# Kernel tuning notes

Measured on AMD Instinct MI355X. Metric: run time of the kernel, lower is better.

Reference implementation:

```python
import jax, jax.numpy as jnp
import numpy as np

EPS = 1e-5


def spmm(rows, cols, vals, x):
    # x: (B, C, V); y[b,c,v] = sum_{e: rows[e]==v} vals[e] * x[b,c,cols[e]]
    B, C, V = x.shape
    xt = x.reshape(B * C, V).T                      # (V, B*C)
    msg = vals[:, None] * xt[cols]                  # (E, B*C)
    y = jax.ops.segment_sum(msg, rows, num_segments=V)
    return y.T.reshape(B, C, V)


def cheb_conv(x, W, b, rows, cols, vals):
    # W: (K, Cin, Cout); Chebyshev recurrence over node dim
    K = W.shape[0]
    Tk = [x]
    if K > 1:
        Tk.append(spmm(rows, cols, vals, x))
    for _ in range(2, K):
        Tk.append(2.0 * spmm(rows, cols, vals, Tk[-1]) - Tk[-2])
    T = jnp.stack(Tk)                               # (K, B, Cin, V)
    out = jnp.einsum('kbiv,kio->bov', T, W)
    if b is not None:
        out = out + b[None, :, None]
    return out


def bn(x, g, be):
    # BatchNorm1d training-mode stats over (batch, nodes) per channel
    m = jnp.mean(x, axis=(0, 2), keepdims=True)
    v = jnp.var(x, axis=(0, 2), keepdims=True)
    return (x - m) * jax.lax.rsqrt(v + EPS) * g[None, :, None] + be[None, :, None]


def res_block(x, rows, cols, vals, ga, bea, Wa, ba, gb, beb, Wb, bb, Ws=None):
    xn = bn(x, ga, bea)
    out = cheb_conv(xn, Wa, ba, rows, cols, vals)
    out = bn(jax.nn.relu(out), gb, beb)
    out = cheb_conv(out, Wb, bb, rows, cols, vals)
    sc = xn if Ws is None else cheb_conv(xn, Ws, None, rows, cols, vals)
    return jax.nn.relu(out + sc)


def setup_inputs() -> dict:
    key = jax.random.key(0)
    ks = iter(jax.random.split(key, 40))
    V, E, B, K = 50000, 800000, 8, 4
    d = {}
    d['x'] = jax.random.normal(next(ks), (B, 16, V), dtype=jnp.float32)
    d['lap_rows'] = jax.random.randint(next(ks), (E,), 0, V, dtype=jnp.int32)
    d['lap_cols'] = jax.random.randint(next(ks), (E,), 0, V, dtype=jnp.int32)
    d['lap_vals'] = jax.random.normal(next(ks), (E,), dtype=jnp.float32) * 0.05

    def w(shape, scale=0.1):
        return jax.random.normal(next(ks), shape, dtype=jnp.float32) * scale

    d['W_in'], d['b_in'] = w((K, 16, 32)), w((32,))
    # block 1: 32 -> [32] -> 32 (identity shortcut)
    d['g1a'], d['be1a'] = jnp.ones(32), jnp.zeros(32)
    d['W1a'], d['b1a'] = w((K, 32, 32)), w((32,))
    d['g1b'], d['be1b'] = jnp.ones(32), jnp.zeros(32)
    d['W1b'], d['b1b'] = w((K, 32, 32)), w((32,))
    # block 2: 32 -> [64] -> 64 (ChebConv K=1 shortcut, no bias)
    d['g2a'], d['be2a'] = jnp.ones(32), jnp.zeros(32)
    d['W2a'], d['b2a'] = w((K, 32, 64)), w((64,))
    d['g2b'], d['be2b'] = jnp.ones(64), jnp.zeros(64)
    d['W2b'], d['b2b'] = w((K, 64, 64)), w((64,))
    d['W2s'] = w((1, 32, 64))
    # block 3: 64 -> [64] -> 64 (identity shortcut)
    d['g3a'], d['be3a'] = jnp.ones(64), jnp.zeros(64)
    d['W3a'], d['b3a'] = w((K, 64, 64)), w((64,))
    d['g3b'], d['be3b'] = jnp.ones(64), jnp.zeros(64)
    d['W3b'], d['b3b'] = w((K, 64, 64)), w((64,))
    # output head
    d['g_out'], d['be_out'] = jnp.ones(64), jnp.zeros(64)
    d['W_out'], d['b_out'] = w((K, 64, 10)), w((10,))
    return d


def reference(x, lap_rows, lap_cols, lap_vals,
              W_in, b_in,
              g1a, be1a, W1a, b1a, g1b, be1b, W1b, b1b,
              g2a, be2a, W2a, b2a, g2b, be2b, W2b, b2b, W2s,
              g3a, be3a, W3a, b3a, g3b, be3b, W3b, b3b,
              g_out, be_out, W_out, b_out):
    r, c, v = lap_rows, lap_cols, lap_vals
    out = jax.nn.relu(cheb_conv(x, W_in, b_in, r, c, v))
    out = res_block(out, r, c, v, g1a, be1a, W1a, b1a, g1b, be1b, W1b, b1b)
    out = res_block(out, r, c, v, g2a, be2a, W2a, b2a, g2b, be2b, W2b, b2b, W2s)
    out = res_block(out, r, c, v, g3a, be3a, W3a, b3a, g3b, be3b, W3b, b3b)
    out = bn(out, g_out, be_out)
    out = jax.nn.relu(cheb_conv(out, W_out, b_out, r, c, v))
    pooled = jnp.max(out, axis=2)                   # global max pool over nodes -> (B, 10)
    return jax.nn.log_softmax(pooled, axis=1)
```

## Files before the change

### kernel.cpp

```cpp
#include <hip/hip_runtime.h>
#include <hip/hip_bf16.h>
#include <hip/hip_fp16.h>

__global__ void hist_kernel(const int* __restrict__ rows, int* __restrict__ counts, int E) {
    int i = blockIdx.x * blockDim.x + threadIdx.x;
    if (i < E) atomicAdd(&counts[rows[i]], 1);
}

__global__ void chunk_sum_kernel(const int* __restrict__ counts, int* __restrict__ chunk_sums, int V) {
    __shared__ int sh[256];
    int t = threadIdx.x;
    int i = blockIdx.x * 256 + t;
    sh[t] = (i < V) ? counts[i] : 0;
    __syncthreads();
    for (int st = 128; st > 0; st >>= 1) {
        if (t < st) sh[t] += sh[t + st];
        __syncthreads();
    }
    if (t == 0) chunk_sums[blockIdx.x] = sh[0];
}

__global__ void scan_chunks_kernel(int* __restrict__ cs, int n) {
    __shared__ int wsum[4];
    int t = threadIdx.x, lane = t & 63, w = t >> 6;
    int orig = (t < n) ? cs[t] : 0;
    int x = orig;
    #pragma unroll
    for (int d = 1; d < 64; d <<= 1) {
        int y = __shfl_up(x, d);
        if (lane >= d) x += y;
    }
    if (lane == 63) wsum[w] = x;
    __syncthreads();
    int wo = 0;
    for (int j = 0; j < w; ++j) wo += wsum[j];
    if (t < n) cs[t] = wo + x - orig;
}

__global__ void scan_final_kernel(const int* __restrict__ counts, const int* __restrict__ chunk_off,
                                  int* __restrict__ row_ptr, int V) {
    __shared__ int wsum[4];
    int t = threadIdx.x, lane = t & 63, w = t >> 6;
    int i = blockIdx.x * 256 + t;
    int x = (i < V) ? counts[i] : 0;
    #pragma unroll
    for (int d = 1; d < 64; d <<= 1) {
        int y = __shfl_up(x, d);
        if (lane >= d) x += y;
    }
    if (lane == 63) wsum[w] = x;
    __syncthreads();
    int wo = 0;
    for (int j = 0; j < w; ++j) wo += wsum[j];
    if (i < V) row_ptr[i + 1] = chunk_off[blockIdx.x] + wo + x;
    if (i == 0) row_ptr[0] = 0;
}

__global__ void init_cursor_kernel(const int* __restrict__ row_ptr, int* __restrict__ cursor, int V) {
    int i = blockIdx.x * blockDim.x + threadIdx.x;
    if (i < V) cursor[i] = row_ptr[i];
}

__global__ void scatter_kernel(const int* __restrict__ rows, const int* __restrict__ cols,
                               const float* __restrict__ vals, int* __restrict__ cursor,
                               int* __restrict__ cols_s, float* __restrict__ vals_s, int E) {
    int i = blockIdx.x * blockDim.x + threadIdx.x;
    if (i < E) {
        int r = rows[i];
        int p = atomicAdd(&cursor[r], 1);
        cols_s[p] = cols[i];
        vals_s[p] = vals[i];
    }
}

__global__ void sort_rows_kernel(const int* __restrict__ row_ptr, int* cols, float* vals, int V) {
    int v = blockIdx.x * blockDim.x + threadIdx.x;
    if (v >= V) return;
    int e0 = row_ptr[v], e1 = row_ptr[v + 1];
    for (int i = e0 + 1; i < e1; ++i) {
        int c = cols[i];
        unsigned xb = __float_as_uint(vals[i]);
        int j = i - 1;
        while (j >= e0) {
            int cj = cols[j];
            unsigned vj = __float_as_uint(vals[j]);
            if (cj > c || (cj == c && vj > xb)) {
                cols[j + 1] = cj; vals[j + 1] = __uint_as_float(vj);
                --j;
            } else break;
        }
        cols[j + 1] = c;
        vals[j + 1] = __uint_as_float(xb);
    }
}

__global__ void transpose_in_kernel(const float* __restrict__ x, __half* __restrict__ X, int V) {
    int total = V * 128;
    for (int i = blockIdx.x * blockDim.x + threadIdx.x; i < total; i += gridDim.x * blockDim.x) {
        int v = i >> 7;
        int t = i & 127;
        X[i] = __float2half(x[t * V + v]);
    }
}

template <int VPT> struct PackT;
template <> struct PackT<1> { using T = float;  };
template <> struct PackT<2> { using T = float2; };
template <> struct PackT<4> { using T = float4; };

template <int VPT>
__global__ __launch_bounds__(256) void spmm2_kernel(
    const int* __restrict__ row_ptr, const int* __restrict__ cols,
    const float* __restrict__ vals, const __half2* __restrict__ src,
    __half2* dst, const __half2* prev, int V) {
    using T = typename PackT<VPT>::T;
    union U { T raw; __half2 h[VPT]; };
    int lane = threadIdx.x & 63;
    int v = (blockIdx.x << 2) | (threadIdx.x >> 6);
    if (v >= V) return;
    const int W = VPT * 64;
    const size_t row = (size_t)v * W + lane * VPT;

    float pr[2 * VPT];
    bool hasp = (prev != nullptr);
    if (hasp) {
        U pv; pv.raw = *(const T*)(prev + row);
        #pragma unroll
        for (int j = 0; j < VPT; ++j) {
            float2 f = __half22float2(pv.h[j]);
            pr[2 * j] = f.x; pr[2 * j + 1] = f.y;
        }
    }
    float acc[2 * VPT];
    #pragma unroll
    for (int j = 0; j < 2 * VPT; ++j) acc[j] = 0.f;

    int e0 = row_ptr[v], e1 = row_ptr[v + 1];
    int e = e0;
    for (; e + 8 <= e1; e += 8) {
        int   c[8]; float w[8]; U g[8];
        #pragma unroll
        for (int k = 0; k < 8; ++k) { c[k] = cols[e + k]; w[k] = vals[e + k]; }
        #pragma unroll
        for (int k = 0; k < 8; ++k)
            g[k].raw = *(const T*)(src + (size_t)c[k] * W + lane * VPT);
        #pragma unroll
        for (int k = 0; k < 8; ++k) {
            #pragma unroll
            for (int j = 0; j < VPT; ++j) {
                float2 f = __half22float2(g[k].h[j]);
                acc[2*j] += w[k] * f.x; acc[2*j+1] += w[k] * f.y;
            }
        }
    }
    for (; e + 4 <= e1; e += 4) {
        int   c[4]; float w[4]; U g[4];
        #pragma unroll
        for (int k = 0; k < 4; ++k) { c[k] = cols[e + k]; w[k] = vals[e + k]; }
        #pragma unroll
        for (int k = 0; k < 4; ++k)
            g[k].raw = *(const T*)(src + (size_t)c[k] * W + lane * VPT);
        #pragma unroll
        for (int k = 0; k < 4; ++k) {
            #pragma unroll
            for (int j = 0; j < VPT; ++j) {
                float2 f = __half22float2(g[k].h[j]);
                acc[2*j] += w[k] * f.x; acc[2*j+1] += w[k] * f.y;
            }
        }
    }
    for (; e < e1; ++e) {
        int c = cols[e]; float wv = vals[e];
        U g; g.raw = *(const T*)(src + (size_t)c * W + lane * VPT);
        #pragma unroll
        for (int j = 0; j < VPT; ++j) {
            float2 f = __half22float2(g.h[j]);
            acc[2*j] += wv * f.x; acc[2*j+1] += wv * f.y;
        }
    }
    if (hasp) {
        #pragma unroll
        for (int j = 0; j < 2 * VPT; ++j) acc[j] = 2.f * acc[j] - pr[j];
    }
    U o;
    #pragma unroll
    for (int j = 0; j < VPT; ++j) o.h[j] = __floats2half2_rn(acc[2*j], acc[2*j+1]);
    *(T*)(dst + row) = o.raw;
}

template <int CIN, int COUT>
__global__ __launch_bounds__(256) void combine_kernel(
    const __half* T0, const __half* T1, const __half* T2, const __half* T3,
    const float* __restrict__ W, const float* __restrict__ bias,
    const __half* res, const __half* sc, const float* __restrict__ Wsc,
    __half* out, int relu, int V) {
    const int CSC = 32;
    int g = blockIdx.x * 256 + threadIdx.x;
    int n = g >> 3, b = g & 7;
    if (n >= V) return;
    size_t ib = (size_t)n * 8 * CIN + (size_t)b * CIN;

    float acc[COUT];
    if (bias) {
        #pragma unroll
        for (int c = 0; c < COUT; ++c) acc[c] = bias[c];
    } else {
        #pragma unroll
        for (int c = 0; c < COUT; ++c) acc[c] = 0.f;
    }

    const __half* Ts[4] = {T0, T1, T2, T3};
    #pragma unroll
    for (int k = 0; k < 4; ++k) {
        const __half2* xr = (const __half2*)(Ts[k] + ib);
        const float* Wk = W + (size_t)k * CIN * COUT;
        for (int q = 0; q < CIN / 2; ++q) {
            float2 x = __half22float2(xr[q]);
            const float* w0 = Wk + (2 * q) * COUT;
            const float* w1 = Wk + (2 * q + 1) * COUT;
            #pragma unroll
            for (int c = 0; c < COUT; ++c) acc[c] = fmaf(x.x, w0[c], acc[c]);
            #pragma unroll
            for (int c = 0; c < COUT; ++c) acc[c] = fmaf(x.y, w1[c], acc[c]);
        }
    }
    if (sc) {
        const __half2* xr = (const __half2*)(sc + (size_t)n * 8 * CSC + (size_t)b * CSC);
        for (int q = 0; q < CSC / 2; ++q) {
            float2 x = __half22float2(xr[q]);
            const float* w0 = Wsc + (2 * q) * COUT;
            const float* w1 = Wsc + (2 * q + 1) * COUT;
            #pragma unroll
            for (int c = 0; c < COUT; ++c) acc[c] = fmaf(x.x, w0[c], acc[c]);
            #pragma unroll
            for (int c = 0; c < COUT; ++c) acc[c] = fmaf(x.y, w1[c], acc[c]);
        }
    }
    size_t ob = (size_t)n * 8 * COUT + (size_t)b * COUT;
    if (res) {
        const __half2* rr = (const __half2*)(res + ob);
        #pragma unroll
        for (int c = 0; c < COUT / 2; ++c) {
            float2 f = __half22float2(rr[c]);
            acc[2 * c] += f.x; acc[2 * c + 1] += f.y;
        }
    }
    if (relu) {
        #pragma unroll
        for (int c = 0; c < COUT; ++c) acc[c] = fmaxf(acc[c], 0.f);
    }
    __half2* ro = (__half2*)(out + ob);
    #pragma unroll
    for (int c = 0; c < COUT / 2; ++c)
        ro[c] = __floats2half2_rn(acc[2 * c], acc[2 * c + 1]);
}

__global__ void bn_stats_part_kernel(const __half* __restrict__ x, int C, int relu_in,
                                     float* __restrict__ part, size_t N) {
    __shared__ float s_sum[256];
    __shared__ float s_sq[256];
    int t = threadIdx.x;
    size_t i0 = (size_t)blockIdx.x * 256 + t;
    size_t step = (size_t)gridDim.x * 256;
    float s = 0.f, q = 0.f;
    for (size_t i = i0; i < N; i += step) {
        float v = __half2float(x[i]);
        if (relu_in) v = fmaxf(v, 0.f);
        s += v; q += v * v;
    }
    s_sum[t] = s; s_sq[t] = q;
    __syncthreads();
    for (int st = 128; st >= C; st >>= 1) {
        if (t < st) { s_sum[t] += s_sum[t + st]; s_sq[t] += s_sq[t + st]; }
        __syncthreads();
    }
    if (t < C) {
        part[blockIdx.x * 128 + t]     = s_sum[t];
        part[blockIdx.x * 128 + C + t] = s_sq[t];
    }
}

__global__ void bn_reduce_kernel(const float* __restrict__ part, int nblk,
                                 const float* __restrict__ g, const float* __restrict__ be,
                                 float* __restrict__ ss, int C, float invN) {
    int c = threadIdx.x;
    if (c < C) {
        float s = 0.f, q = 0.f;
        for (int b = 0; b < nblk; ++b) {
            s += part[b * 128 + c];
            q += part[b * 128 + C + c];
        }
        float m = s * invN;
        float var = q * invN - m * m;
        float sc = g[c] * rsqrtf(var + 1e-5f);
        ss[c] = sc;
        ss[C + c] = be[c] - m * sc;
    }
}

__global__ void affine_h_kernel(__half* x, const float* __restrict__ ss, int C,
                                int relu_in, size_t N) {
    size_t stride = (size_t)gridDim.x * blockDim.x;
    for (size_t i = (size_t)blockIdx.x * blockDim.x + threadIdx.x; i < N; i += stride) {
        int c = (int)(i & (size_t)(C - 1));
        float v = __half2float(x[i]);
        if (relu_in) v = fmaxf(v, 0.f);
        x[i] = __float2half(v * ss[c] + ss[C + c]);
    }
}

__global__ void maxpool_h_kernel(const __half* __restrict__ x, float* __restrict__ pooled, int V) {
    __shared__ float red[256];
    int o = blockIdx.x;
    float m = 0.f;
    for (int v = threadIdx.x; v < V; v += 256)
        m = fmaxf(m, __half2float(x[(size_t)v * 80 + o]));
    red[threadIdx.x] = m;
    __syncthreads();
    for (int st = 128; st > 0; st >>= 1) {
        if (threadIdx.x < st) red[threadIdx.x] = fmaxf(red[threadIdx.x], red[threadIdx.x + st]);
        __syncthreads();
    }
    if (threadIdx.x == 0) pooled[o] = red[0];
}

__global__ void lsm_kernel(const float* __restrict__ pooled, float* __restrict__ out) {
    int b = threadIdx.x;
    if (b < 8) {
        float m = -1e30f;
        for (int c = 0; c < 10; ++c) m = fmaxf(m, pooled[b * 10 + c]);
        float s = 0.f;
        for (int c = 0; c < 10; ++c) s += expf(pooled[b * 10 + c] - m);
        float l = logf(s);
        for (int c = 0; c < 10; ++c)
            out[b * 10 + c] = pooled[b * 10 + c] - m - l;
    }
}

__global__ void encode_kernel(float* out, float val) {
    int i = threadIdx.x;
    if (i < 80) out[i] = val;
}

extern "C" void kernel_launch(void* const* d_in, const int* in_sizes, int n_in,
                              void* d_out, int out_size, void* d_ws, size_t ws_size,
                              hipStream_t stream) {
    (void)in_sizes; (void)n_in; (void)out_size;
    const int V = 50000, E = 800000;
    const int NCH = (V + 255) / 256;
    const int SB = 256;

    auto al = [](size_t x) { return (x + 255) & ~(size_t)255; };
    const size_t FB = al((size_t)V * 512 * sizeof(__half));
    const size_t need = 5 * FB + al((V + 1) * 4) + al(V * 4) + al(E * 4) + al(E * 4)
                      + al(SB * 128 * 4) + al(8 * 128 * 4) + al(80 * 4) + al(NCH * 4);
    if (ws_size < need) {
        encode_kernel<<<1, 128, 0, stream>>>((float*)d_out, (float)(ws_size >> 20));
        return;
    }

    const float* x_in = (const float*)d_in[0];
    const int* rows   = (const int*)d_in[1];
    const int* colsi  = (const int*)d_in[2];
    const float* lvals = (const float*)d_in[3];
    const float* W_in = (const float*)d_in[4];
    const float* b_in = (const float*)d_in[5];
    const float* g1a = (const float*)d_in[6],  *be1a = (const float*)d_in[7];
    const float* W1a = (const float*)d_in[8],  *b1a  = (const float*)d_in[9];
    const float* g1b = (const float*)d_in[10], *be1b = (const float*)d_in[11];
    const float* W1b = (const float*)d_in[12], *b1b  = (const float*)d_in[13];
    const float* g2a = (const float*)d_in[14], *be2a = (const float*)d_in[15];
    const float* W2a = (const float*)d_in[16], *b2a  = (const float*)d_in[17];
    const float* g2b = (const float*)d_in[18], *be2b = (const float*)d_in[19];
    const float* W2b = (const float*)d_in[20], *b2b  = (const float*)d_in[21];
    const float* W2s = (const float*)d_in[22];
    const float* g3a = (const float*)d_in[23], *be3a = (const float*)d_in[24];
    const float* W3a = (const float*)d_in[25], *b3a  = (const float*)d_in[26];
    const float* g3b = (const float*)d_in[27], *be3b = (const float*)d_in[28];
    const float* W3b = (const float*)d_in[29], *b3b  = (const float*)d_in[30];
    const float* g_o = (const float*)d_in[31], *be_o = (const float*)d_in[32];
    const float* W_o = (const float*)d_in[33], *b_o  = (const float*)d_in[34];

    char* wp = (char*)d_ws;
    auto take = [&](size_t bytes) -> void* { void* p = (void*)wp; wp += al(bytes); return p; };
    __half* P0 = (__half*)take(FB);
    __half* P1 = (__half*)take(FB);
    __half* P2 = (__half*)take(FB);
    __half* P3 = (__half*)take(FB);
    __half* P4 = (__half*)take(FB);
    int* row_ptr  = (int*)take((V + 1) * sizeof(int));
    int* cursor   = (int*)take(V * sizeof(int));
    int* cols_s   = (int*)take(E * sizeof(int));
    float* vals_s = (float*)take(E * sizeof(float));
    float* part   = (float*)take(SB * 128 * sizeof(float));
    float* aff    = (float*)take(8 * 128 * sizeof(float));
    float* pooled = (float*)take(80 * sizeof(float));
    int* chunks   = (int*)take(NCH * sizeof(int));

    hipMemsetAsync(d_ws, 0, need, stream);

    hist_kernel<<<(E + 255) / 256, 256, 0, stream>>>(rows, cursor, E);
    chunk_sum_kernel<<<NCH, 256, 0, stream>>>(cursor, chunks, V);
    scan_chunks_kernel<<<1, 256, 0, stream>>>(chunks, NCH);
    scan_final_kernel<<<NCH, 256, 0, stream>>>(cursor, chunks, row_ptr, V);
    init_cursor_kernel<<<(V + 255) / 256, 256, 0, stream>>>(row_ptr, cursor, V);
    scatter_kernel<<<(E + 255) / 256, 256, 0, stream>>>(rows, colsi, lvals, cursor, cols_s, vals_s, E);
    sort_rows_kernel<<<(V + 255) / 256, 256, 0, stream>>>(row_ptr, cols_s, vals_s, V);
    transpose_in_kernel<<<4096, 256, 0, stream>>>(x_in, P0, V);

    auto spmm = [&](const __half* src, __half* dst, const __half* prev, int C) {
        int grid = (V + 3) / 4;
        if (C == 16)
            spmm2_kernel<1><<<grid, 256, 0, stream>>>(row_ptr, cols_s, vals_s,
                (const __half2*)src, (__half2*)dst, (const __half2*)prev, V);
        else if (C == 32)
            spmm2_kernel<2><<<grid, 256, 0, stream>>>(row_ptr, cols_s, vals_s,
                (const __half2*)src, (__half2*)dst, (const __half2*)prev, V);
        else
            spmm2_kernel<4><<<grid, 256, 0, stream>>>(row_ptr, cols_s, vals_s,
                (const __half2*)src, (__half2*)dst, (const __half2*)prev, V);
    };
    const int MG = (V * 8 + 255) / 256;
    auto comb = [&](const __half* T0, const __half* T1, const __half* T2, const __half* T3,
                    int Cin, int Cout, const float* W, const float* bias,
                    const __half* res, const __half* sc, const float* Wsc,
                    __half* out, int relu) {
        if (Cin == 16 && Cout == 32)
            combine_kernel<16, 32><<<MG, 256, 0, stream>>>(T0, T1, T2, T3, W, bias, res, sc, Wsc, out, relu, V);
        else if (Cin == 32 && Cout == 32)
            combine_kernel<32, 32><<<MG, 256, 0, stream>>>(T0, T1, T2, T3, W, bias, res, sc, Wsc, out, relu, V);
        else if (Cin == 32 && Cout == 64)
            combine_kernel<32, 64><<<MG, 256, 0, stream>>>(T0, T1, T2, T3, W, bias, res, sc, Wsc, out, relu, V);
        else if (Cin == 64 && Cout == 64)
            combine_kernel<64, 64><<<MG, 256, 0, stream>>>(T0, T1, T2, T3, W, bias, res, sc, Wsc, out, relu, V);
        else
            combine_kernel<64, 10><<<MG, 256, 0, stream>>>(T0, T1, T2, T3, W, bias, res, sc, Wsc, out, relu, V);
    };
    auto stats = [&](const __half* xb, int C, int relu, int slot, const float* g, const float* be) {
        bn_stats_part_kernel<<<SB, 256, 0, stream>>>(xb, C, relu, part, (size_t)V * 8 * C);
        bn_reduce_kernel<<<1, 64, 0, stream>>>(part, SB, g, be, aff + slot * 128, C,
                                               1.f / ((float)V * 8.f));
    };
    auto affine = [&](__half* xb, int C, int relu, int slot) {
        affine_h_kernel<<<2048, 256, 0, stream>>>(xb, aff + slot * 128, C, relu, (size_t)V * 8 * C);
    };
    const __half* NH = nullptr;
    const float*  NF = nullptr;

    spmm(P0, P1, nullptr, 16);
    spmm(P1, P2, P0, 16);
    spmm(P2, P3, P1, 16);
    comb(P0, P1, P2, P3, 16, 32, W_in, b_in, NH, NH, NF, P4, 1);

    stats(P4, 32, 0, 0, g1a, be1a);
    affine(P4, 32, 0, 0);
    spmm(P4, P0, nullptr, 32);
    spmm(P0, P1, P4, 32);
    spmm(P1, P2, P0, 32);
    comb(P4, P0, P1, P2, 32, 32, W1a, b1a, NH, NH, NF, P0, 0);
    stats(P0, 32, 1, 1, g1b, be1b);
    affine(P0, 32, 1, 1);
    spmm(P0, P1, nullptr, 32);
    spmm(P1, P2, P0, 32);
    spmm(P2, P3, P1, 32);
    comb(P0, P1, P2, P3, 32, 32, W1b, b1b, P4, NH, NF, P4, 1);

    stats(P4, 32, 0, 2, g2a, be2a);
    affine(P4, 32, 0, 2);
    spmm(P4, P0, nullptr, 32);
    spmm(P0, P1, P4, 32);
    spmm(P1, P2, P0, 32);
    comb(P4, P0, P1, P2, 32, 64, W2a, b2a, NH, NH, NF, P3, 0);
    stats(P3, 64, 1, 3, g2b, be2b);
    affine(P3, 64, 1, 3);
    spmm(P3, P0, nullptr, 64);
    spmm(P0, P1, P3, 64);
    spmm(P1, P2, P0, 64);
    comb(P3, P0, P1, P2, 64, 64, W2b, b2b, NH, P4, W2s, P0, 1);

    stats(P0, 64, 0, 4, g3a, be3a);
    affine(P0, 64, 0, 4);
    spmm(P0, P1, nullptr, 64);
    spmm(P1, P2, P0, 64);
    spmm(P2, P3, P1, 64);
    comb(P0, P1, P2, P3, 64, 64, W3a, b3a, NH, NH, NF, P1, 0);
    stats(P1, 64, 1, 5, g3b, be3b);
    affine(P1, 64, 1, 5);
    spmm(P1, P2, nullptr, 64);
    spmm(P2, P3, P1, 64);
    spmm(P3, P4, P2, 64);
    comb(P1, P2, P3, P4, 64, 64, W3b, b3b, P0, NH, NF, P1, 1);

    stats(P1, 64, 0, 6, g_o, be_o);
    affine(P1, 64, 0, 6);
    spmm(P1, P0, nullptr, 64);
    spmm(P0, P2, P1, 64);
    spmm(P2, P3, P0, 64);
    comb(P1, P0, P2, P3, 64, 10, W_o, b_o, NH, NH, NF, P4, 1);
    maxpool_h_kernel<<<80, 256, 0, stream>>>(P4, pooled, V);
    lsm_kernel<<<1, 64, 0, stream>>>(pooled, (float*)d_out);
}
```

Baseline: 4.897 ms.

## Process two rows per thread in combine, vectorize affine, split maxpool, trim memset

The combine kernel now computes two batch rows per thread with float4 input loads, so each weight load is reused twice. The affine kernel is vectorized to half2, and maxpool is split across node slices that merge with an integer atomicMax on non-negative floats. Batch-norm stats use more blocks, and the full workspace memset is replaced by zeroing only the cursor and pooled buffers. The costs are higher register pressure in combine and a reliance on pooled values being non-negative.

```diff
diff --git a/kernel.cpp b/kernel.cpp
--- a/kernel.cpp
+++ b/kernel.cpp
@@ -195,64 +195,100 @@
     const __half* res, const __half* sc, const float* __restrict__ Wsc,
     __half* out, int relu, int V) {
     const int CSC = 32;
+    union U4 { float4 raw; __half2 h[4]; };
     int g = blockIdx.x * 256 + threadIdx.x;
-    int n = g >> 3, b = g & 7;
-    if (n >= V) return;
+    int r0 = 2 * g;
+    if (r0 >= V * 8) return;
+    int n = r0 >> 3, b = r0 & 7;
     size_t ib = (size_t)n * 8 * CIN + (size_t)b * CIN;
 
-    float acc[COUT];
-    if (bias) {
-        #pragma unroll
-        for (int c = 0; c < COUT; ++c) acc[c] = bias[c];
-    } else {
-        #pragma unroll
-        for (int c = 0; c < COUT; ++c) acc[c] = 0.f;
+    float acc0[COUT], acc1[COUT];
+    #pragma unroll
+    for (int c = 0; c < COUT; ++c) {
+        float bb = bias ? bias[c] : 0.f;
+        acc0[c] = bb; acc1[c] = bb;
     }
 
     const __half* Ts[4] = {T0, T1, T2, T3};
     #pragma unroll
     for (int k = 0; k < 4; ++k) {
-        const __half2* xr = (const __half2*)(Ts[k] + ib);
+        const float4* rp0 = (const float4*)(Ts[k] + ib);
+        const float4* rp1 = (const float4*)(Ts[k] + ib + CIN);
         const float* Wk = W + (size_t)k * CIN * COUT;
-        for (int q = 0; q < CIN / 2; ++q) {
-            float2 x = __half22float2(xr[q]);
-            const float* w0 = Wk + (2 * q) * COUT;
-            const float* w1 = Wk + (2 * q + 1) * COUT;
+        for (int c4 = 0; c4 < CIN / 8; ++c4) {
+            U4 x0, x1;
+            x0.raw = rp0[c4];
+            x1.raw = rp1[c4];
             #pragma unroll
-            for (int c = 0; c < COUT; ++c) acc[c] = fmaf(x.x, w0[c], acc[c]);
+            for (int s = 0; s < 4; ++s) {
+                int q = c4 * 4 + s;
+                float2 a0 = __half22float2(x0.h[s]);
+                float2 a1 = __half22float2(x1.h[s]);
+                const float* w0 = Wk + (2 * q) * COUT;
+                const float* w1 = Wk + (2 * q + 1) * COUT;
+                #pragma unroll
+                for (int c = 0; c < COUT; ++c) {
+                    float wv0 = w0[c], wv1 = w1[c];
+                    acc0[c] = fmaf(a0.x, wv0, acc0[c]);
+                    acc0[c] = fmaf(a0.y, wv1, acc0[c]);
+                    acc1[c] = fmaf(a1.x, wv0, acc1[c]);
+                    acc1[c] = fmaf(a1.y, wv1, acc1[c]);
+                }
+            }
+        }
+    }
+    if (sc) {
+        size_t sb = (size_t)n * 8 * CSC + (size_t)b * CSC;
+        const float4* sp0 = (const float4*)(sc + sb);
+        const float4* sp1 = (const float4*)(sc + sb + CSC);
+        for (int c4 = 0; c4 < CSC / 8; ++c4) {
+            U4 x0, x1;
+            x0.raw = sp0[c4];
+            x1.raw = sp1[c4];
             #pragma unroll
-            for (int c = 0; c < COUT; ++c) acc[c] = fmaf(x.y, w1[c], acc[c]);
-        }
-    }
-    if (sc) {
-        const __half2* xr = (const __half2*)(sc + (size_t)n * 8 * CSC + (size_t)b * CSC);
-        for (int q = 0; q < CSC / 2; ++q) {
-            float2 x = __half22float2(xr[q]);
-            const float* w0 = Wsc + (2 * q) * COUT;
-            const float* w1 = Wsc + (2 * q + 1) * COUT;
-            #pragma unroll
-            for (int c = 0; c < COUT; ++c) acc[c] = fmaf(x.x, w0[c], acc[c]);
-            #pragma unroll
-            for (int c = 0; c < COUT; ++c) acc[c] = fmaf(x.y, w1[c], acc[c]);
+            for (int s = 0; s < 4; ++s) {
+                int q = c4 * 4 + s;
+                float2 a0 = __half22float2(x0.h[s]);
+                float2 a1 = __half22float2(x1.h[s]);
+                const float* w0 = Wsc + (2 * q) * COUT;
+                const float* w1 = Wsc + (2 * q + 1) * COUT;
+                #pragma unroll
+                for (int c = 0; c < COUT; ++c) {
+                    float wv0 = w0[c], wv1 = w1[c];
+                    acc0[c] = fmaf(a0.x, wv0, acc0[c]);
+                    acc0[c] = fmaf(a0.y, wv1, acc0[c]);
+                    acc1[c] = fmaf(a1.x, wv0, acc1[c]);
+                    acc1[c] = fmaf(a1.y, wv1, acc1[c]);
+                }
+            }
         }
     }
     size_t ob = (size_t)n * 8 * COUT + (size_t)b * COUT;
     if (res) {
-        const __half2* rr = (const __half2*)(res + ob);
+        const __half2* rr0 = (const __half2*)(res + ob);
+        const __half2* rr1 = (const __half2*)(res + ob + COUT);
         #pragma unroll
         for (int c = 0; c < COUT / 2; ++c) {
-            float2 f = __half22float2(rr[c]);
-            acc[2 * c] += f.x; acc[2 * c + 1] += f.y;
+            float2 f0 = __half22float2(rr0[c]);
+            float2 f1 = __half22float2(rr1[c]);
+            acc0[2*c] += f0.x; acc0[2*c+1] += f0.y;
+            acc1[2*c] += f1.x; acc1[2*c+1] += f1.y;
         }
     }
     if (relu) {
         #pragma unroll
-        for (int c = 0; c < COUT; ++c) acc[c] = fmaxf(acc[c], 0.f);
-    }
-    __half2* ro = (__half2*)(out + ob);
-    #pragma unroll
-    for (int c = 0; c < COUT / 2; ++c)
-        ro[c] = __floats2half2_rn(acc[2 * c], acc[2 * c + 1]);
+        for (int c = 0; c < COUT; ++c) {
+            acc0[c] = fmaxf(acc0[c], 0.f);
+            acc1[c] = fmaxf(acc1[c], 0.f);
+        }
+    }
+    __half2* ro0 = (__half2*)(out + ob);
+    __half2* ro1 = (__half2*)(out + ob + COUT);
+    #pragma unroll
+    for (int c = 0; c < COUT / 2; ++c) {
+        ro0[c] = __floats2half2_rn(acc0[2*c], acc0[2*c+1]);
+        ro1[c] = __floats2half2_rn(acc1[2*c], acc1[2*c+1]);
+    }
 }
 
 __global__ void bn_stats_part_kernel(const __half* __restrict__ x, int C, int relu_in,
@@ -299,21 +335,27 @@
 }
 
 __global__ void affine_h_kernel(__half* x, const float* __restrict__ ss, int C,
-                                int relu_in, size_t N) {
+                                int relu_in, size_t N2) {
     size_t stride = (size_t)gridDim.x * blockDim.x;
-    for (size_t i = (size_t)blockIdx.x * blockDim.x + threadIdx.x; i < N; i += stride) {
-        int c = (int)(i & (size_t)(C - 1));
-        float v = __half2float(x[i]);
-        if (relu_in) v = fmaxf(v, 0.f);
-        x[i] = __float2half(v * ss[c] + ss[C + c]);
-    }
-}
-
-__global__ void maxpool_h_kernel(const __half* __restrict__ x, float* __restrict__ pooled, int V) {
+    __half2* x2 = (__half2*)x;
+    for (size_t i = (size_t)blockIdx.x * blockDim.x + threadIdx.x; i < N2; i += stride) {
+        int c0 = (int)((2 * i) & (size_t)(C - 1));
+        float2 f = __half22float2(x2[i]);
+        if (relu_in) { f.x = fmaxf(f.x, 0.f); f.y = fmaxf(f.y, 0.f); }
+        f.x = f.x * ss[c0] + ss[C + c0];
+        f.y = f.y * ss[c0 + 1] + ss[C + c0 + 1];
+        x2[i] = __floats2half2_rn(f.x, f.y);
+    }
+}
+
+__global__ void maxpool_h_kernel(const __half* __restrict__ x, float* pooled, int V, int NS) {
     __shared__ float red[256];
-    int o = blockIdx.x;
+    int o = blockIdx.x % 80;
+    int slice = blockIdx.x / 80;
+    int v0 = (int)((long long)V * slice / NS);
+    int v1 = (int)((long long)V * (slice + 1) / NS);
     float m = 0.f;
-    for (int v = threadIdx.x; v < V; v += 256)
+    for (int v = v0 + threadIdx.x; v < v1; v += 256)
         m = fmaxf(m, __half2float(x[(size_t)v * 80 + o]));
     red[threadIdx.x] = m;
     __syncthreads();
@@ -321,7 +363,7 @@
         if (threadIdx.x < st) red[threadIdx.x] = fmaxf(red[threadIdx.x], red[threadIdx.x + st]);
         __syncthreads();
     }
-    if (threadIdx.x == 0) pooled[o] = red[0];
+    if (threadIdx.x == 0) atomicMax((int*)&pooled[o], __float_as_int(red[0]));
 }
 
 __global__ void lsm_kernel(const float* __restrict__ pooled, float* __restrict__ out) {
@@ -348,12 +390,13 @@
     (void)in_sizes; (void)n_in; (void)out_size;
     const int V = 50000, E = 800000;
     const int NCH = (V + 255) / 256;
-    const int SB = 256;
+    const int SB = 1024;
+    const int NS = 8;
 
     auto al = [](size_t x) { return (x + 255) & ~(size_t)255; };
     const size_t FB = al((size_t)V * 512 * sizeof(__half));
     const size_t need = 5 * FB + al((V + 1) * 4) + al(V * 4) + al(E * 4) + al(E * 4)
-                      + al(SB * 128 * 4) + al(8 * 128 * 4) + al(80 * 4) + al(NCH * 4);
+                      + al((size_t)SB * 128 * 4) + al(8 * 128 * 4) + al(80 * 4) + al(NCH * 4);
     if (ws_size < need) {
         encode_kernel<<<1, 128, 0, stream>>>((float*)d_out, (float)(ws_size >> 20));
         return;
@@ -392,12 +435,13 @@
     int* cursor   = (int*)take(V * sizeof(int));
     int* cols_s   = (int*)take(E * sizeof(int));
     float* vals_s = (float*)take(E * sizeof(float));
-    float* part   = (float*)take(SB * 128 * sizeof(float));
+    float* part   = (float*)take((size_t)SB * 128 * sizeof(float));
     float* aff    = (float*)take(8 * 128 * sizeof(float));
     float* pooled = (float*)take(80 * sizeof(float));
     int* chunks   = (int*)take(NCH * sizeof(int));
 
-    hipMemsetAsync(d_ws, 0, need, stream);
+    hipMemsetAsync(cursor, 0, V * sizeof(int), stream);
+    hipMemsetAsync(pooled, 0, 80 * sizeof(float), stream);
 
     hist_kernel<<<(E + 255) / 256, 256, 0, stream>>>(rows, cursor, E);
     chunk_sum_kernel<<<NCH, 256, 0, stream>>>(cursor, chunks, V);
@@ -420,21 +464,21 @@
             spmm2_kernel<4><<<grid, 256, 0, stream>>>(row_ptr, cols_s, vals_s,
                 (const __half2*)src, (__half2*)dst, (const __half2*)prev, V);
     };
-    const int MG = (V * 8 + 255) / 256;
+    const int MG2 = (V * 8 / 2 + 255) / 256;
     auto comb = [&](const __half* T0, const __half* T1, const __half* T2, const __half* T3,
                     int Cin, int Cout, const float* W, const float* bias,
                     const __half* res, const __half* sc, const float* Wsc,
                     __half* out, int relu) {
         if (Cin == 16 && Cout == 32)
-            combine_kernel<16, 32><<<MG, 256, 0, stream>>>(T0, T1, T2, T3, W, bias, res, sc, Wsc, out, relu, V);
+            combine_kernel<16, 32><<<MG2, 256, 0, stream>>>(T0, T1, T2, T3, W, bias, res, sc, Wsc, out, relu, V);
         else if (Cin == 32 && Cout == 32)
-            combine_kernel<32, 32><<<MG, 256, 0, stream>>>(T0, T1, T2, T3, W, bias, res, sc, Wsc, out, relu, V);
+            combine_kernel<32, 32><<<MG2, 256, 0, stream>>>(T0, T1, T2, T3, W, bias, res, sc, Wsc, out, relu, V);
         else if (Cin == 32 && Cout == 64)
-            combine_kernel<32, 64><<<MG, 256, 0, stream>>>(T0, T1, T2, T3, W, bias, res, sc, Wsc, out, relu, V);
+            combine_kernel<32, 64><<<MG2, 256, 0, stream>>>(T0, T1, T2, T3, W, bias, res, sc, Wsc, out, relu, V);
         else if (Cin == 64 && Cout == 64)
-            combine_kernel<64, 64><<<MG, 256, 0, stream>>>(T0, T1, T2, T3, W, bias, res, sc, Wsc, out, relu, V);
+            combine_kernel<64, 64><<<MG2, 256, 0, stream>>>(T0, T1, T2, T3, W, bias, res, sc, Wsc, out, relu, V);
         else
-            combine_kernel<64, 10><<<MG, 256, 0, stream>>>(T0, T1, T2, T3, W, bias, res, sc, Wsc, out, relu, V);
+            combine_kernel<64, 10><<<MG2, 256, 0, stream>>>(T0, T1, T2, T3, W, bias, res, sc, Wsc, out, relu, V);
     };
     auto stats = [&](const __half* xb, int C, int relu, int slot, const float* g, const float* be) {
         bn_stats_part_kernel<<<SB, 256, 0, stream>>>(xb, C, relu, part, (size_t)V * 8 * C);
@@ -442,7 +486,8 @@
                                                1.f / ((float)V * 8.f));
     };
     auto affine = [&](__half* xb, int C, int relu, int slot) {
-        affine_h_kernel<<<2048, 256, 0, stream>>>(xb, aff + slot * 128, C, relu, (size_t)V * 8 * C);
+        affine_h_kernel<<<2048, 256, 0, stream>>>(xb, aff + slot * 128, C, relu,
+                                                  (size_t)V * 4 * C);
     };
     const __half* NH = nullptr;
     const float*  NF = nullptr;
@@ -497,6 +542,6 @@
     spmm(P0, P2, P1, 64);
     spmm(P2, P3, P0, 64);
     comb(P1, P0, P2, P3, 64, 10, W_o, b_o, NH, NH, NF, P4, 1);
-    maxpool_h_kernel<<<80, 256, 0, stream>>>(P4, pooled, V);
+    maxpool_h_kernel<<<80 * NS, 256, 0, stream>>>(P4, pooled, V, NS);
     lsm_kernel<<<1, 64, 0, stream>>>(pooled, (float*)d_out);
 }
```

Measured after the change: 5.839 ms. 19.2% more time.

## Vectorize combine and affine loads, shrink memset, split maxpool with atomics

Applied to the files above, without the earlier changes.

The combine kernel now reads its half-precision inputs as float4 vectors and interleaves the two FMAs per channel pair. The affine BN kernel processes half2 pairs per thread. The full-workspace memset is replaced by small memsets of only the cursor and pooled buffers. Global max pooling is split over node slices and merged with an integer atomicMax, which is valid only because the inputs are non-negative after ReLU and pooled starts at zero.

```diff
diff --git a/kernel.cpp b/kernel.cpp
--- a/kernel.cpp
+++ b/kernel.cpp
@@ -195,45 +195,55 @@
     const __half* res, const __half* sc, const float* __restrict__ Wsc,
     __half* out, int relu, int V) {
     const int CSC = 32;
+    union U4 { float4 raw; __half2 h[4]; };
     int g = blockIdx.x * 256 + threadIdx.x;
+    if (g >= V * 8) return;
     int n = g >> 3, b = g & 7;
-    if (n >= V) return;
     size_t ib = (size_t)n * 8 * CIN + (size_t)b * CIN;
 
     float acc[COUT];
-    if (bias) {
-        #pragma unroll
-        for (int c = 0; c < COUT; ++c) acc[c] = bias[c];
-    } else {
-        #pragma unroll
-        for (int c = 0; c < COUT; ++c) acc[c] = 0.f;
-    }
+    #pragma unroll
+    for (int c = 0; c < COUT; ++c) acc[c] = bias ? bias[c] : 0.f;
 
     const __half* Ts[4] = {T0, T1, T2, T3};
     #pragma unroll
     for (int k = 0; k < 4; ++k) {
-        const __half2* xr = (const __half2*)(Ts[k] + ib);
+        const float4* rp = (const float4*)(Ts[k] + ib);
         const float* Wk = W + (size_t)k * CIN * COUT;
-        for (int q = 0; q < CIN / 2; ++q) {
-            float2 x = __half22float2(xr[q]);
-            const float* w0 = Wk + (2 * q) * COUT;
-            const float* w1 = Wk + (2 * q + 1) * COUT;
+        #pragma unroll
+        for (int c4 = 0; c4 < CIN / 8; ++c4) {
+            U4 x; x.raw = rp[c4];
             #pragma unroll
-            for (int c = 0; c < COUT; ++c) acc[c] = fmaf(x.x, w0[c], acc[c]);
+            for (int s = 0; s < 4; ++s) {
+                int q = c4 * 4 + s;
+                float2 a = __half22float2(x.h[s]);
+                const float* w0 = Wk + (2 * q) * COUT;
+                const float* w1 = Wk + (2 * q + 1) * COUT;
+                #pragma unroll
+                for (int c = 0; c < COUT; ++c) {
+                    acc[c] = fmaf(a.x, w0[c], acc[c]);
+                    acc[c] = fmaf(a.y, w1[c], acc[c]);
+                }
+            }
+        }
+    }
+    if (sc) {
+        const float4* sp = (const float4*)(sc + (size_t)n * 8 * CSC + (size_t)b * CSC);
+        #pragma unroll
+        for (int c4 = 0; c4 < CSC / 8; ++c4) {
+            U4 x; x.raw = sp[c4];
             #pragma unroll
-            for (int c = 0; c < COUT; ++c) acc[c] = fmaf(x.y, w1[c], acc[c]);
-        }
-    }
-    if (sc) {
-        const __half2* xr = (const __half2*)(sc + (size_t)n * 8 * CSC + (size_t)b * CSC);
-        for (int q = 0; q < CSC / 2; ++q) {
-            float2 x = __half22float2(xr[q]);
-            const float* w0 = Wsc + (2 * q) * COUT;
-            const float* w1 = Wsc + (2 * q + 1) * COUT;
-            #pragma unroll
-            for (int c = 0; c < COUT; ++c) acc[c] = fmaf(x.x, w0[c], acc[c]);
-            #pragma unroll
-            for (int c = 0; c < COUT; ++c) acc[c] = fmaf(x.y, w1[c], acc[c]);
+            for (int s = 0; s < 4; ++s) {
+                int q = c4 * 4 + s;
+                float2 a = __half22float2(x.h[s]);
+                const float* w0 = Wsc + (2 * q) * COUT;
+                const float* w1 = Wsc + (2 * q + 1) * COUT;
+                #pragma unroll
+                for (int c = 0; c < COUT; ++c) {
+                    acc[c] = fmaf(a.x, w0[c], acc[c]);
+                    acc[c] = fmaf(a.y, w1[c], acc[c]);
+                }
+            }
         }
     }
     size_t ob = (size_t)n * 8 * COUT + (size_t)b * COUT;
@@ -299,21 +309,27 @@
 }
 
 __global__ void affine_h_kernel(__half* x, const float* __restrict__ ss, int C,
-                                int relu_in, size_t N) {
+                                int relu_in, size_t N2) {
     size_t stride = (size_t)gridDim.x * blockDim.x;
-    for (size_t i = (size_t)blockIdx.x * blockDim.x + threadIdx.x; i < N; i += stride) {
-        int c = (int)(i & (size_t)(C - 1));
-        float v = __half2float(x[i]);
-        if (relu_in) v = fmaxf(v, 0.f);
-        x[i] = __float2half(v * ss[c] + ss[C + c]);
-    }
-}
-
-__global__ void maxpool_h_kernel(const __half* __restrict__ x, float* __restrict__ pooled, int V) {
+    __half2* x2 = (__half2*)x;
+    for (size_t i = (size_t)blockIdx.x * blockDim.x + threadIdx.x; i < N2; i += stride) {
+        int c0 = (int)((2 * i) & (size_t)(C - 1));
+        float2 f = __half22float2(x2[i]);
+        if (relu_in) { f.x = fmaxf(f.x, 0.f); f.y = fmaxf(f.y, 0.f); }
+        f.x = f.x * ss[c0] + ss[C + c0];
+        f.y = f.y * ss[c0 + 1] + ss[C + c0 + 1];
+        x2[i] = __floats2half2_rn(f.x, f.y);
+    }
+}
+
+__global__ void maxpool_h_kernel(const __half* __restrict__ x, float* pooled, int V, int NS) {
     __shared__ float red[256];
-    int o = blockIdx.x;
+    int o = blockIdx.x % 80;
+    int slice = blockIdx.x / 80;
+    int v0 = (int)((long long)V * slice / NS);
+    int v1 = (int)((long long)V * (slice + 1) / NS);
     float m = 0.f;
-    for (int v = threadIdx.x; v < V; v += 256)
+    for (int v = v0 + threadIdx.x; v < v1; v += 256)
         m = fmaxf(m, __half2float(x[(size_t)v * 80 + o]));
     red[threadIdx.x] = m;
     __syncthreads();
@@ -321,7 +337,7 @@
         if (threadIdx.x < st) red[threadIdx.x] = fmaxf(red[threadIdx.x], red[threadIdx.x + st]);
         __syncthreads();
     }
-    if (threadIdx.x == 0) pooled[o] = red[0];
+    if (threadIdx.x == 0) atomicMax((int*)&pooled[o], __float_as_int(red[0]));
 }
 
 __global__ void lsm_kernel(const float* __restrict__ pooled, float* __restrict__ out) {
@@ -349,11 +365,12 @@
     const int V = 50000, E = 800000;
     const int NCH = (V + 255) / 256;
     const int SB = 256;
+    const int NS = 8;
 
     auto al = [](size_t x) { return (x + 255) & ~(size_t)255; };
     const size_t FB = al((size_t)V * 512 * sizeof(__half));
     const size_t need = 5 * FB + al((V + 1) * 4) + al(V * 4) + al(E * 4) + al(E * 4)
-                      + al(SB * 128 * 4) + al(8 * 128 * 4) + al(80 * 4) + al(NCH * 4);
+                      + al((size_t)SB * 128 * 4) + al(8 * 128 * 4) + al(80 * 4) + al(NCH * 4);
     if (ws_size < need) {
         encode_kernel<<<1, 128, 0, stream>>>((float*)d_out, (float)(ws_size >> 20));
         return;
@@ -392,12 +409,13 @@
     int* cursor   = (int*)take(V * sizeof(int));
     int* cols_s   = (int*)take(E * sizeof(int));
     float* vals_s = (float*)take(E * sizeof(float));
-    float* part   = (float*)take(SB * 128 * sizeof(float));
+    float* part   = (float*)take((size_t)SB * 128 * sizeof(float));
     float* aff    = (float*)take(8 * 128 * sizeof(float));
     float* pooled = (float*)take(80 * sizeof(float));
     int* chunks   = (int*)take(NCH * sizeof(int));
 
-    hipMemsetAsync(d_ws, 0, need, stream);
+    hipMemsetAsync(cursor, 0, V * sizeof(int), stream);
+    hipMemsetAsync(pooled, 0, 80 * sizeof(float), stream);
 
     hist_kernel<<<(E + 255) / 256, 256, 0, stream>>>(rows, cursor, E);
     chunk_sum_kernel<<<NCH, 256, 0, stream>>>(cursor, chunks, V);
@@ -442,7 +460,8 @@
                                                1.f / ((float)V * 8.f));
     };
     auto affine = [&](__half* xb, int C, int relu, int slot) {
-        affine_h_kernel<<<2048, 256, 0, stream>>>(xb, aff + slot * 128, C, relu, (size_t)V * 8 * C);
+        affine_h_kernel<<<2048, 256, 0, stream>>>(xb, aff + slot * 128, C, relu,
+                                                  (size_t)V * 4 * C);
     };
     const __half* NH = nullptr;
     const float*  NF = nullptr;
@@ -497,6 +516,6 @@
     spmm(P0, P2, P1, 64);
     spmm(P2, P3, P0, 64);
     comb(P1, P0, P2, P3, 64, 10, W_o, b_o, NH, NH, NF, P4, 1);
-    maxpool_h_kernel<<<80, 256, 0, stream>>>(P4, pooled, V);
+    maxpool_h_kernel<<<80 * NS, 256, 0, stream>>>(P4, pooled, V, NS);
     lsm_kernel<<<1, 64, 0, stream>>>(pooled, (float*)d_out);
 }
```

New measurement: 4.584 ms. -6.4%, faster.
